# Performance work log

Hardware: AMD Instinct MI355X
Metric: run time of the kernel (lower is better)

The kernel has to match this reference:

```python
import jax, jax.numpy as jnp
import numpy as np

D_MODEL = 512
N_HEADS = 8
HEAD_DIM = D_MODEL // N_HEADS
MAX_LEN = 250  # relative table has 2*MAX_LEN-1 = 499 rows
B, L = 2, 2048


def setup_inputs() -> dict:
    rng = jax.random.key(0)
    ks = jax.random.split(rng, 10)
    w = 1.0 / np.sqrt(D_MODEL)
    return {
        "query": jax.random.normal(ks[0], (B, L, D_MODEL), jnp.float32),
        "key": jax.random.normal(ks[1], (B, L, D_MODEL), jnp.float32),
        "value": jax.random.normal(ks[2], (B, L, D_MODEL), jnp.float32),
        "mask": jax.random.randint(ks[3], (B, L), 0, 2, jnp.int32),
        # weights stored as [in, out]; apply as x @ W + b (equivalent to torch Linear)
        "Wq": jax.random.normal(ks[4], (D_MODEL, D_MODEL), jnp.float32) * w,
        "bq": jnp.zeros((D_MODEL,), jnp.float32),
        "Wk": jax.random.normal(ks[5], (D_MODEL, D_MODEL), jnp.float32) * w,
        "bk": jnp.zeros((D_MODEL,), jnp.float32),
        "Wv": jax.random.normal(ks[6], (D_MODEL, D_MODEL), jnp.float32) * w,
        "bv": jnp.zeros((D_MODEL,), jnp.float32),
        "Wo": jax.random.normal(ks[7], (D_MODEL, D_MODEL), jnp.float32) * w,
        "bo": jnp.zeros((D_MODEL,), jnp.float32),
        "rel_table": jax.random.normal(ks[8], (2 * MAX_LEN - 1, HEAD_DIM), jnp.float32),
    }


def reference(query, key, value, mask, Wq, bq, Wk, bk, Wv, bv, Wo, bo, rel_table):
    b, l, d = query.shape
    hd = d // N_HEADS

    def split_heads(x):  # [b,l,d] -> [b,h,l,hd]
        return x.reshape(b, l, N_HEADS, hd).transpose(0, 2, 1, 3)

    Q = split_heads(query @ Wq + bq)
    K = split_heads(key @ Wk + bk)
    V = split_heads(value @ Wv + bv)

    scores = jnp.einsum('bhid,bhjd->bhij', Q, K) / jnp.sqrt(jnp.float32(hd))

    # relative position indices: idx[i,j] = clamp(j - i + MAX_LEN-1, 0, 2*MAX_LEN-2)
    pos = jnp.arange(l)
    idx = jnp.clip(pos[None, :] - pos[:, None] + MAX_LEN - 1, 0, 2 * MAX_LEN - 2)
    rel = rel_table[idx]  # [l, l, hd] gather
    # Shaw-style additive relative-position bias (per-pair scalar from Q . rel)
    scores = scores + jnp.einsum('bhid,ijd->bhij', Q, rel)

    # key-padding mask: [b,l] -> [b,1,1,l]
    scores = jnp.where(mask[:, None, None, :] == 0, jnp.float32(-1e10), scores)

    weights = jax.nn.softmax(scores, axis=-1)  # [b,h,l,l]
    out = jnp.einsum('bhij,bhjd->bhid', weights, V)
    out = out.transpose(0, 2, 1, 3).reshape(b, l, d)
    return out @ Wo + bo
```

## Files before the change

### kernel.cpp

```cpp
#include <hip/hip_runtime.h>
#include <math.h>

#define NREL 499
#define NREL_PAD 504
#define LDB 72
#define LDT 72

typedef __attribute__((ext_vector_type(8))) short bf16x8;
typedef __attribute__((ext_vector_type(4))) float f32x4;

__device__ __forceinline__ float bf2f(ushort x) {
  union { unsigned u; float f; } v; v.u = ((unsigned)x) << 16; return v.f;
}
__device__ __forceinline__ ushort f2bf(float x) {
  union { float f; unsigned u; } v; v.f = x;
  return (ushort)((v.u + 0x8000u) >> 16);
}
__device__ __forceinline__ ushort f2h(float x) {
  union { _Float16 h; ushort u; } v; v.h = (_Float16)x; return v.u;
}
__device__ __forceinline__ float h2f(ushort u) {
  union { _Float16 h; ushort u; } v; v.u = u; return (float)v.h;
}
__device__ __forceinline__ bf16x8 pack8(float4 a, float4 b) {
  bf16x8 r;
  r[0] = (short)f2bf(a.x); r[1] = (short)f2bf(a.y);
  r[2] = (short)f2bf(a.z); r[3] = (short)f2bf(a.w);
  r[4] = (short)f2bf(b.x); r[5] = (short)f2bf(b.y);
  r[6] = (short)f2bf(b.z); r[7] = (short)f2bf(b.w);
  return r;
}

__global__ __launch_bounds__(256) void prep_wt(const float* __restrict__ W0,
                                               const float* __restrict__ W1,
                                               const float* __restrict__ W2,
                                               const float* __restrict__ W3,
                                               const int* __restrict__ mask,
                                               const float* __restrict__ rel,
                                               ushort* __restrict__ Wt,
                                               ushort* __restrict__ maskbf,
                                               ushort* __restrict__ rel8) {
  __shared__ float T[64][68];
  const int t = threadIdx.x;
  const int k0 = blockIdx.x * 64, n0 = blockIdx.y * 64, z = blockIdx.z;
  const float* W = (z == 0) ? W0 : (z == 1) ? W1 : (z == 2) ? W2 : W3;
#pragma unroll
  for (int s = 0; s < 4; ++s) {
    int idx = t + s * 256;
    int r = idx >> 4, c4 = (idx & 15) << 2;
    *(float4*)&T[r][c4] = *(const float4*)(W + (size_t)(k0 + r) * 512 + n0 + c4);
  }
  if (blockIdx.x == 0 && blockIdx.y == 0) {
    int base = z * 1024 + t * 4;
    int4 mv = *(const int4*)(mask + base);
    ushort4 mo;
    mo.x = mv.x ? 0x3F80 : 0; mo.y = mv.y ? 0x3F80 : 0;
    mo.z = mv.z ? 0x3F80 : 0; mo.w = mv.w ? 0x3F80 : 0;
    *(ushort4*)(maskbf + base) = mo;
  } else if (blockIdx.x == 1 && blockIdx.y == 0) {
    int base = z * 8192 + t * 32;
#pragma unroll
    for (int c = 0; c < 4; ++c) {
      int e0 = base + c * 8;
      ushort tmp[8];
#pragma unroll
      for (int k = 0; k < 8; ++k) {
        int e = e0 + k;
        float v = (e < NREL * 64) ? rel[e] * 8.f : 0.f;
        tmp[k] = f2bf(v);
      }
      *(ushort4*)(rel8 + e0) = make_ushort4(tmp[0], tmp[1], tmp[2], tmp[3]);
      *(ushort4*)(rel8 + e0 + 4) = make_ushort4(tmp[4], tmp[5], tmp[6], tmp[7]);
    }
  }
  __syncthreads();
#pragma unroll
  for (int s = 0; s < 4; ++s) {
    int idx = t + s * 256;
    int row = idx >> 4, c4 = (idx & 15) << 2;
    ushort4 u = make_ushort4(f2bf(T[c4 + 0][row]), f2bf(T[c4 + 1][row]),
                             f2bf(T[c4 + 2][row]), f2bf(T[c4 + 3][row]));
    *(ushort4*)(Wt + (size_t)z * 262144 + (size_t)(n0 + row) * 512 + k0 + c4) = u;
  }
}

template <int MODE, int AFP32>
__device__ __forceinline__ void gemm_tile_body(const void* __restrict__ Av,
                                               const ushort* __restrict__ Wt,
                                               const float* __restrict__ bias,
                                               const int* __restrict__ mvec,
                                               void* __restrict__ outv,
                                               int bx, int by, float oscale) {
  __shared__ ushort As[64 * LDT];
  __shared__ ushort Bs[64 * LDT];
  const int t = threadIdx.x;
  const int lane = t & 63, wave = t >> 6;
  const int m16 = lane & 15, quad = lane >> 4;
  const int koff = quad << 3;
  const int i0 = by * 64, n0 = bx * 64;
  const int row0 = t >> 3, off0 = (t & 7) << 3;
  const int row1 = (t + 256) >> 3, off1 = ((t + 256) & 7) << 3;
  const ushort* Ab16 = (const ushort*)Av + (size_t)i0 * 512;
  const float*  Ab32 = (const float*)Av + (size_t)i0 * 512;
  const ushort* Bb = Wt + (size_t)n0 * 512;

  uint4 ar0, ar1;
  float4 af00, af01, af10, af11;
  if (AFP32) {
    af00 = *(const float4*)(Ab32 + (size_t)row0 * 512 + off0);
    af01 = *(const float4*)(Ab32 + (size_t)row0 * 512 + off0 + 4);
    af10 = *(const float4*)(Ab32 + (size_t)row1 * 512 + off1);
    af11 = *(const float4*)(Ab32 + (size_t)row1 * 512 + off1 + 4);
  } else {
    ar0 = *(const uint4*)(Ab16 + (size_t)row0 * 512 + off0);
    ar1 = *(const uint4*)(Ab16 + (size_t)row1 * 512 + off1);
  }
  uint4 br0 = *(const uint4*)(Bb + (size_t)row0 * 512 + off0);
  uint4 br1 = *(const uint4*)(Bb + (size_t)row1 * 512 + off1);

  f32x4 acc[4] = {{0.f, 0.f, 0.f, 0.f}, {0.f, 0.f, 0.f, 0.f},
                  {0.f, 0.f, 0.f, 0.f}, {0.f, 0.f, 0.f, 0.f}};

  for (int ks = 0; ks < 8; ++ks) {
    __syncthreads();
    if (AFP32) {
      *(bf16x8*)&As[row0 * LDT + off0] = pack8(af00, af01);
      *(bf16x8*)&As[row1 * LDT + off1] = pack8(af10, af11);
    } else {
      *(uint4*)&As[row0 * LDT + off0] = ar0;
      *(uint4*)&As[row1 * LDT + off1] = ar1;
    }
    *(uint4*)&Bs[row0 * LDT + off0] = br0;
    *(uint4*)&Bs[row1 * LDT + off1] = br1;
    __syncthreads();

    const int kn = ((ks + 1) & 7) << 6;
    if (AFP32) {
      af00 = *(const float4*)(Ab32 + (size_t)row0 * 512 + kn + off0);
      af01 = *(const float4*)(Ab32 + (size_t)row0 * 512 + kn + off0 + 4);
      af10 = *(const float4*)(Ab32 + (size_t)row1 * 512 + kn + off1);
      af11 = *(const float4*)(Ab32 + (size_t)row1 * 512 + kn + off1 + 4);
    } else {
      ar0 = *(const uint4*)(Ab16 + (size_t)row0 * 512 + kn + off0);
      ar1 = *(const uint4*)(Ab16 + (size_t)row1 * 512 + kn + off1);
    }
    br0 = *(const uint4*)(Bb + (size_t)row0 * 512 + kn + off0);
    br1 = *(const uint4*)(Bb + (size_t)row1 * 512 + kn + off1);

    __builtin_amdgcn_s_setprio(1);
    if (MODE != 1) {
#pragma unroll
      for (int kh = 0; kh < 2; ++kh) {
        bf16x8 af = *(const bf16x8*)&As[((wave << 4) + m16) * LDT + (kh << 5) + koff];
#pragma unroll
        for (int nt = 0; nt < 4; ++nt) {
          bf16x8 wf = *(const bf16x8*)&Bs[((nt << 4) + m16) * LDT + (kh << 5) + koff];
          acc[nt] = __builtin_amdgcn_mfma_f32_16x16x32_bf16(af, wf, acc[nt], 0, 0, 0);
        }
      }
    } else {
#pragma unroll
      for (int kh = 0; kh < 2; ++kh) {
        bf16x8 wf = *(const bf16x8*)&Bs[((wave << 4) + m16) * LDT + (kh << 5) + koff];
#pragma unroll
        for (int it = 0; it < 4; ++it) {
          bf16x8 af = *(const bf16x8*)&As[((it << 4) + m16) * LDT + (kh << 5) + koff];
          acc[it] = __builtin_amdgcn_mfma_f32_16x16x32_bf16(wf, af, acc[it], 0, 0, 0);
        }
      }
    }
    __builtin_amdgcn_s_setprio(0);
  }

  if (MODE == 0) {
    float* out = (float*)outv;
#pragma unroll
    for (int nt = 0; nt < 4; ++nt) {
      float bn = bias[n0 + (nt << 4) + m16];
#pragma unroll
      for (int r = 0; r < 4; ++r) {
        int i = i0 + (wave << 4) + (quad << 2) + r;
        out[(size_t)i * 512 + n0 + (nt << 4) + m16] = acc[nt][r] + bn;
      }
    }
  } else {
    ushort* out = (ushort*)outv;
    const int b = i0 >> 11, l0 = i0 & 2047, h = n0 >> 6;
    float4 b4 = *(const float4*)(bias + n0 + (wave << 4) + (quad << 2));
    float bb[4] = {b4.x, b4.y, b4.z, b4.w};
    float mkf[4];
#pragma unroll
    for (int it = 0; it < 4; ++it)
      mkf[it] = (mvec[b * 2048 + l0 + (it << 4) + m16] != 0) ? 1.f : 0.f;
#pragma unroll
    for (int r = 0; r < 4; ++r) {
      int d = (wave << 4) + (quad << 2) + r;
#pragma unroll
      for (int it = 0; it < 4; ++it) {
        out[((size_t)(b * 8 + h) * 64 + d) * 2048 + l0 + (it << 4) + m16] =
            f2bf((acc[it][r] + bb[r]) * mkf[it]);
      }
    }
  }
}

template <int MODE, int AFP32>
__global__ __launch_bounds__(256) void gemm_tile(const void* __restrict__ A,
                                                 const ushort* __restrict__ Wt,
                                                 const float* __restrict__ bias,
                                                 void* __restrict__ outv) {
  gemm_tile_body<MODE, AFP32>(A, Wt, bias, nullptr, outv, blockIdx.x,
                              blockIdx.y, 1.f);
}

__device__ __forceinline__ void gemm_qk128(const float* __restrict__ A,
                                           const ushort* __restrict__ Wt,
                                           const float* __restrict__ bias,
                                           ushort* __restrict__ out,
                                           int bx, int by, float oscale) {
  __shared__ ushort As[128 * LDT];
  __shared__ ushort Bs[64 * LDT];
  const int t = threadIdx.x;
  const int lane = t & 63, wave = t >> 6;
  const int m16 = lane & 15, quad = lane >> 4;
  const int koff = quad << 3;
  const int i0 = by * 128, n0 = bx * 64;
  const float* Ab = A + (size_t)i0 * 512;
  const ushort* Bb = Wt + (size_t)n0 * 512;

  int arow[4], acol[4];
#pragma unroll
  for (int s = 0; s < 4; ++s) {
    int idx = t + s * 256;
    arow[s] = idx >> 3;
    acol[s] = (idx & 7) << 3;
  }
  const int brow0 = t >> 3, bcol0 = (t & 7) << 3;
  const int brow1 = (t + 256) >> 3, bcol1 = ((t + 256) & 7) << 3;

  float4 afA[4], afB[4];
  uint4 br0, br1;
#pragma unroll
  for (int s = 0; s < 4; ++s) {
    afA[s] = *(const float4*)(Ab + (size_t)arow[s] * 512 + acol[s]);
    afB[s] = *(const float4*)(Ab + (size_t)arow[s] * 512 + acol[s] + 4);
  }
  br0 = *(const uint4*)(Bb + (size_t)brow0 * 512 + bcol0);
  br1 = *(const uint4*)(Bb + (size_t)brow1 * 512 + bcol1);

  f32x4 acc[2][4];
#pragma unroll
  for (int mi = 0; mi < 2; ++mi)
#pragma unroll
    for (int nt = 0; nt < 4; ++nt) acc[mi][nt] = (f32x4){0.f, 0.f, 0.f, 0.f};

  for (int ks = 0; ks < 8; ++ks) {
    __syncthreads();
#pragma unroll
    for (int s = 0; s < 4; ++s)
      *(bf16x8*)&As[arow[s] * LDT + acol[s]] = pack8(afA[s], afB[s]);
    *(uint4*)&Bs[brow0 * LDT + bcol0] = br0;
    *(uint4*)&Bs[brow1 * LDT + bcol1] = br1;
    __syncthreads();

    const int kn = ((ks + 1) & 7) << 6;
#pragma unroll
    for (int s = 0; s < 4; ++s) {
      afA[s] = *(const float4*)(Ab + (size_t)arow[s] * 512 + kn + acol[s]);
      afB[s] = *(const float4*)(Ab + (size_t)arow[s] * 512 + kn + acol[s] + 4);
    }
    br0 = *(const uint4*)(Bb + (size_t)brow0 * 512 + kn + bcol0);
    br1 = *(const uint4*)(Bb + (size_t)brow1 * 512 + kn + bcol1);

    __builtin_amdgcn_s_setprio(1);
#pragma unroll
    for (int kh = 0; kh < 2; ++kh) {
      bf16x8 af0 = *(const bf16x8*)&As[((wave << 5) + m16) * LDT + (kh << 5) + koff];
      bf16x8 af1 = *(const bf16x8*)&As[((wave << 5) + 16 + m16) * LDT + (kh << 5) + koff];
#pragma unroll
      for (int nt = 0; nt < 4; ++nt) {
        bf16x8 wf = *(const bf16x8*)&Bs[((nt << 4) + m16) * LDT + (kh << 5) + koff];
        acc[0][nt] = __builtin_amdgcn_mfma_f32_16x16x32_bf16(af0, wf, acc[0][nt], 0, 0, 0);
        acc[1][nt] = __builtin_amdgcn_mfma_f32_16x16x32_bf16(af1, wf, acc[1][nt], 0, 0, 0);
      }
    }
    __builtin_amdgcn_s_setprio(0);
  }

  const int b = i0 >> 11, l0 = i0 & 2047, h = n0 >> 6;
#pragma unroll
  for (int nt = 0; nt < 4; ++nt) {
    float bn = bias[n0 + (nt << 4) + m16];
    int d = (nt << 4) + m16;
#pragma unroll
    for (int mi = 0; mi < 2; ++mi) {
#pragma unroll
      for (int r = 0; r < 4; ++r) {
        int il = (wave << 5) + (mi << 4) + (quad << 2) + r;
        out[((size_t)(b * 8 + h) * 2048 + l0 + il) * 64 + d] =
            f2bf((acc[mi][nt][r] + bn) * oscale);
      }
    }
  }
}

__global__ __launch_bounds__(256) void gemm_qkv(
    const float* __restrict__ q, const float* __restrict__ k,
    const float* __restrict__ v, const ushort* __restrict__ Wt,
    const float* __restrict__ bq, const float* __restrict__ bk,
    const float* __restrict__ bv, const int* __restrict__ mask,
    ushort* __restrict__ Qw, ushort* __restrict__ Kw, ushort* __restrict__ Vtw) {
  const int z = blockIdx.z;
  if (z == 0) {
    gemm_qk128(q, Wt, bq, Qw, blockIdx.x, blockIdx.y, 0.125f);
  } else if (z == 1) {
    gemm_qk128(k, Wt + 262144, bk, Kw, blockIdx.x, blockIdx.y, 1.f);
  } else {
#pragma unroll
    for (int s = 0; s < 2; ++s)
      gemm_tile_body<1, 1>(v, Wt + 2 * 262144, bv, mask, (void*)Vtw,
                           blockIdx.x, blockIdx.y * 2 + s, 1.f);
  }
}

__global__ __launch_bounds__(256) void qrel_tile(const ushort* __restrict__ Qw,
                                                 const ushort* __restrict__ rel8,
                                                 ushort* __restrict__ qrelh) {
  __shared__ ushort As[64 * LDT];
  __shared__ ushort Bs[64 * LDT];
  const int t = threadIdx.x;
  const int lane = t & 63, wave = t >> 6;
  const int m16 = lane & 15, quad = lane >> 4;
  const int koff = quad << 3;
  const int r0 = blockIdx.x * 64;
  const int i0 = blockIdx.y * 64;
  const int bh = blockIdx.z;
  const int row0 = t >> 3, off0 = (t & 7) << 3;
  const int row1 = (t + 256) >> 3, off1 = ((t + 256) & 7) << 3;

  *(uint4*)&As[row0 * LDT + off0] =
      *(const uint4*)(Qw + ((size_t)bh * 2048 + i0 + row0) * 64 + off0);
  *(uint4*)&As[row1 * LDT + off1] =
      *(const uint4*)(Qw + ((size_t)bh * 2048 + i0 + row1) * 64 + off1);
  *(uint4*)&Bs[row0 * LDT + off0] =
      *(const uint4*)(rel8 + (size_t)(r0 + row0) * 64 + off0);
  *(uint4*)&Bs[row1 * LDT + off1] =
      *(const uint4*)(rel8 + (size_t)(r0 + row1) * 64 + off1);
  __syncthreads();

  f32x4 acc[4] = {{0.f, 0.f, 0.f, 0.f}, {0.f, 0.f, 0.f, 0.f},
                  {0.f, 0.f, 0.f, 0.f}, {0.f, 0.f, 0.f, 0.f}};
#pragma unroll
  for (int kh = 0; kh < 2; ++kh) {
    bf16x8 af = *(const bf16x8*)&As[((wave << 4) + m16) * LDT + (kh << 5) + koff];
#pragma unroll
    for (int nt = 0; nt < 4; ++nt) {
      bf16x8 wf = *(const bf16x8*)&Bs[((nt << 4) + m16) * LDT + (kh << 5) + koff];
      acc[nt] = __builtin_amdgcn_mfma_f32_16x16x32_bf16(af, wf, acc[nt], 0, 0, 0);
    }
  }

  __syncthreads();
#pragma unroll
  for (int nt = 0; nt < 4; ++nt) {
#pragma unroll
    for (int rg = 0; rg < 4; ++rg) {
      int il = (wave << 4) + (quad << 2) + rg;
      As[il * LDT + (nt << 4) + m16] = f2h(acc[nt][rg]);
    }
  }
  __syncthreads();

  const int orow = t >> 2, och = (t & 3) << 4;
  uint4 s0 = *(const uint4*)&As[orow * LDT + och];
  uint4 s1 = *(const uint4*)&As[orow * LDT + och + 8];
  ushort* dst = qrelh + ((size_t)bh * 2048 + i0 + orow) * NREL_PAD + r0 + och;
  *(uint4*)dst = s0;
  if (r0 + och + 15 < NREL_PAD) *(uint4*)(dst + 8) = s1;
}

__device__ __forceinline__ void gather_qv(float qv[4][4],
                                          const ushort* __restrict__ qrow,
                                          float e_lo, float e_hi,
                                          int iq, int iw0, int j0, int quad) {
  if (j0 - iw0 >= 264) {
#pragma unroll
    for (int jt = 0; jt < 4; ++jt)
#pragma unroll
      for (int r = 0; r < 4; ++r) qv[jt][r] = e_hi;
  } else if (iw0 - j0 >= 312) {
#pragma unroll
    for (int jt = 0; jt < 4; ++jt)
#pragma unroll
      for (int r = 0; r < 4; ++r) qv[jt][r] = e_lo;
  } else {
#pragma unroll
    for (int jt = 0; jt < 4; ++jt) {
#pragma unroll
      for (int r = 0; r < 4; ++r) {
        int j = j0 + (jt << 4) + (quad << 2) + r;
        int rr = min(NREL - 1, max(0, j - iq + 249));
        qv[jt][r] = h2f(qrow[rr]);
      }
    }
  }
}

__global__ __launch_bounds__(256) void flash_attn(
    const ushort* __restrict__ Qw, const ushort* __restrict__ Kw,
    const ushort* __restrict__ Vt, const ushort* __restrict__ qrelh,
    const ushort* __restrict__ maskbf, ushort* __restrict__ attnbf) {
  __shared__ ushort QPs[64 * LDB];
  __shared__ ushort Ks[64 * LDB];
  __shared__ ushort Vs[64 * LDB];
  const int t = threadIdx.x;
  const int lane = t & 63, wave = t >> 6;
  const int m16 = lane & 15, quad = lane >> 4;
  const int koff = quad << 3;
  const int bid = ((int)blockIdx.y << 5) + (int)blockIdx.x;
  const int swz = ((bid & 7) << 6) + (bid >> 3);
  const int i0 = (swz & 31) << 6;
  const int bh = swz >> 5;
  const int b = bh >> 3, h = bh & 7;
  const ushort* Qb = Qw + (size_t)bh * 2048 * 64;
  const ushort* Kb = Kw + (size_t)bh * 2048 * 64;
  const ushort* Vb = Vt + (size_t)bh * 64 * 2048;
  const ushort* mbf = maskbf + b * 2048;
  const int iw0 = i0 + (wave << 4);
  const int iq = iw0 + m16;
  const ushort* qrow = qrelh + ((size_t)bh * 2048 + iq) * NREL_PAD;
  const float e_lo = h2f(qrow[0]), e_hi = h2f(qrow[NREL - 1]);

  const int row0 = t >> 3, off0 = (t & 7) << 3;
  const int row1 = (t + 256) >> 3, off1 = ((t + 256) & 7) << 3;

  *(uint4*)&QPs[row0 * LDB + off0] =
      *(const uint4*)(Qb + (size_t)(i0 + row0) * 64 + off0);
  *(uint4*)&QPs[row1 * LDB + off1] =
      *(const uint4*)(Qb + (size_t)(i0 + row1) * 64 + off1);
  __syncthreads();

  bf16x8 qa0 = *(const bf16x8*)&QPs[((wave << 4) + m16) * LDB + koff];
  bf16x8 qa1 = *(const bf16x8*)&QPs[((wave << 4) + m16) * LDB + 32 + koff];

  float m_i = -INFINITY;
  f32x4 oacc[4];
  f32x4 lacc = {0.f, 0.f, 0.f, 0.f};
#pragma unroll
  for (int dt = 0; dt < 4; ++dt) oacc[dt] = (f32x4){0.f, 0.f, 0.f, 0.f};

  uint4 krA0 = *(const uint4*)(Kb + (size_t)row0 * 64 + off0);
  uint4 krA1 = *(const uint4*)(Kb + (size_t)row1 * 64 + off1);
  uint4 vrA0 = *(const uint4*)(Vb + (size_t)row0 * 2048 + off0);
  uint4 vrA1 = *(const uint4*)(Vb + (size_t)row1 * 2048 + off1);
  bf16x8 mfA0 = *(const bf16x8*)(mbf + koff);
  bf16x8 mfA1 = *(const bf16x8*)(mbf + 32 + koff);
  float qvA[4][4];
  gather_qv(qvA, qrow, e_lo, e_hi, iq, iw0, 0, quad);
  uint4 krB0, krB1, vrB0, vrB1;
  bf16x8 mfB0, mfB1;
  float qvB[4][4];

#define FLASH_STEP(KR0, KR1, VR0, VR1, MF0, MF1, QV,                          \
                   KN0, KN1, VN0, VN1, MG0, MG1, QN, JN)                      \
  do {                                                                        \
    __syncthreads();                                                          \
    *(uint4*)&Ks[row0 * LDB + off0] = KR0;                                    \
    *(uint4*)&Ks[row1 * LDB + off1] = KR1;                                    \
    *(uint4*)&Vs[row0 * LDB + off0] = VR0;                                    \
    *(uint4*)&Vs[row1 * LDB + off1] = VR1;                                    \
    __syncthreads();                                                          \
    KN0 = *(const uint4*)(Kb + (size_t)((JN) + row0) * 64 + off0);            \
    KN1 = *(const uint4*)(Kb + (size_t)((JN) + row1) * 64 + off1);            \
    VN0 = *(const uint4*)(Vb + (size_t)row0 * 2048 + (JN) + off0);            \
    VN1 = *(const uint4*)(Vb + (size_t)row1 * 2048 + (JN) + off1);            \
    MG0 = *(const bf16x8*)(mbf + (JN) + koff);                                \
    MG1 = *(const bf16x8*)(mbf + (JN) + 32 + koff);                           \
    gather_qv(QN, qrow, e_lo, e_hi, iq, iw0, (JN), quad);                     \
    f32x4 sacc[4];                                                            \
    __builtin_amdgcn_s_setprio(1);                                            \
    _Pragma("unroll")                                                         \
    for (int jt = 0; jt < 4; ++jt) {                                          \
      bf16x8 kf0 = *(const bf16x8*)&Ks[((jt << 4) + m16) * LDB + koff];       \
      bf16x8 kf1 = *(const bf16x8*)&Ks[((jt << 4) + m16) * LDB + 32 + koff];  \
      f32x4 z = {QV[jt][0], QV[jt][1], QV[jt][2], QV[jt][3]};                 \
      z = __builtin_amdgcn_mfma_f32_16x16x32_bf16(kf0, qa0, z, 0, 0, 0);      \
      z = __builtin_amdgcn_mfma_f32_16x16x32_bf16(kf1, qa1, z, 0, 0, 0);      \
      sacc[jt] = z;                                                           \
    }                                                                         \
    __builtin_amdgcn_s_setprio(0);                                            \
    float t0 = fmaxf(fmaxf(sacc[0][0], sacc[0][1]),                           \
                     fmaxf(sacc[0][2], sacc[0][3]));                          \
    float t1 = fmaxf(fmaxf(sacc[1][0], sacc[1][1]),                           \
                     fmaxf(sacc[1][2], sacc[1][3]));                          \
    float t2 = fmaxf(fmaxf(sacc[2][0], sacc[2][1]),                           \
                     fmaxf(sacc[2][2], sacc[2][3]));                          \
    float t3 = fmaxf(fmaxf(sacc[3][0], sacc[3][1]),                           \
                     fmaxf(sacc[3][2], sacc[3][3]));                          \
    float mx = fmaxf(fmaxf(t0, t1), fmaxf(t2, t3));                           \
    mx = fmaxf(mx, __shfl_xor(mx, 16));                                       \
    mx = fmaxf(mx, __shfl_xor(mx, 32));                                       \
    if (__any(mx > m_i + 8.f)) {                                              \
      float mnew = fmaxf(m_i, mx);                                            \
      float al = __expf(m_i - mnew);                                          \
      m_i = mnew;                                                             \
      _Pragma("unroll")                                                       \
      for (int dt = 0; dt < 4; ++dt) {                                        \
        oacc[dt][0] *= al; oacc[dt][1] *= al;                                 \
        oacc[dt][2] *= al; oacc[dt][3] *= al;                                 \
      }                                                                       \
      lacc[0] *= al; lacc[1] *= al; lacc[2] *= al; lacc[3] *= al;             \
    }                                                                         \
    const int prow = ((wave << 4) + m16) * LDB;                               \
    _Pragma("unroll")                                                         \
    for (int jt = 0; jt < 4; ++jt) {                                          \
      ushort4 pk;                                                             \
      pk.x = f2bf(__expf(sacc[jt][0] - m_i));                                 \
      pk.y = f2bf(__expf(sacc[jt][1] - m_i));                                 \
      pk.z = f2bf(__expf(sacc[jt][2] - m_i));                                 \
      pk.w = f2bf(__expf(sacc[jt][3] - m_i));                                 \
      *(ushort4*)&QPs[prow + (jt << 4) + (quad << 2)] = pk;                   \
    }                                                                         \
    __asm__ volatile("s_waitcnt lgkmcnt(0)" ::: "memory");                    \
    bf16x8 pa0 = *(const bf16x8*)&QPs[prow + koff];                           \
    bf16x8 pa1 = *(const bf16x8*)&QPs[prow + 32 + koff];                      \
    __builtin_amdgcn_s_setprio(1);                                            \
    lacc = __builtin_amdgcn_mfma_f32_16x16x32_bf16(MF0, pa0, lacc, 0, 0, 0);  \
    lacc = __builtin_amdgcn_mfma_f32_16x16x32_bf16(MF1, pa1, lacc, 0, 0, 0);  \
    _Pragma("unroll")                                                         \
    for (int dt = 0; dt < 4; ++dt) {                                          \
      bf16x8 vf0 = *(const bf16x8*)&Vs[((dt << 4) + m16) * LDB + koff];       \
      bf16x8 vf1 = *(const bf16x8*)&Vs[((dt << 4) + m16) * LDB + 32 + koff];  \
      oacc[dt] =                                                              \
          __builtin_amdgcn_mfma_f32_16x16x32_bf16(vf0, pa0, oacc[dt], 0, 0, 0); \
      oacc[dt] =                                                              \
          __builtin_amdgcn_mfma_f32_16x16x32_bf16(vf1, pa1, oacc[dt], 0, 0, 0); \
    }                                                                         \
    __builtin_amdgcn_s_setprio(0);                                            \
  } while (0)

  for (int j0 = 0; j0 < 2048; j0 += 128) {
    FLASH_STEP(krA0, krA1, vrA0, vrA1, mfA0, mfA1, qvA,
               krB0, krB1, vrB0, vrB1, mfB0, mfB1, qvB, j0 + 64);
    FLASH_STEP(krB0, krB1, vrB0, vrB1, mfB0, mfB1, qvB,
               krA0, krA1, vrA0, vrA1, mfA0, mfA1, qvA, (j0 + 128) & 2047);
  }
#undef FLASH_STEP

  float inv = 1.0f / lacc[0];
  ushort* dst = attnbf + (size_t)(b * 2048 + iq) * 512 + h * 64;
#pragma unroll
  for (int dt = 0; dt < 4; ++dt) {
    ushort4 st;
    st.x = f2bf(oacc[dt][0] * inv);
    st.y = f2bf(oacc[dt][1] * inv);
    st.z = f2bf(oacc[dt][2] * inv);
    st.w = f2bf(oacc[dt][3] * inv);
    *(ushort4*)(dst + (dt << 4) + (quad << 2)) = st;
  }
}

extern "C" void kernel_launch(void* const* d_in, const int* in_sizes, int n_in,
                              void* d_out, int out_size, void* d_ws,
                              size_t ws_size, hipStream_t stream) {
  const float* query = (const float*)d_in[0];
  const float* key   = (const float*)d_in[1];
  const float* value = (const float*)d_in[2];
  const int*   mask  = (const int*)d_in[3];
  const float* Wq = (const float*)d_in[4];
  const float* bq = (const float*)d_in[5];
  const float* Wk = (const float*)d_in[6];
  const float* bk = (const float*)d_in[7];
  const float* Wv = (const float*)d_in[8];
  const float* bv = (const float*)d_in[9];
  const float* Wo = (const float*)d_in[10];
  const float* bo = (const float*)d_in[11];
  const float* rel = (const float*)d_in[12];

  char* w = (char*)d_ws;
  size_t off = 0;
  ushort* Qw  = (ushort*)(w + off); off += (size_t)16 * 2048 * 64 * 2;
  ushort* Kw  = (ushort*)(w + off); off += (size_t)16 * 2048 * 64 * 2;
  ushort* Vtw = (ushort*)(w + off); off += (size_t)16 * 64 * 2048 * 2;
  ushort* Wt  = (ushort*)(w + off); off += (size_t)4 * 512 * 512 * 2;
  ushort* qrelh = (ushort*)(w + off); off += (size_t)16 * 2048 * NREL_PAD * 2;
  ushort* attnbf = (ushort*)(w + off); off += (size_t)4096 * 512 * 2;
  ushort* maskbf = (ushort*)(w + off); off += (size_t)2 * 2048 * 2;
  ushort* rel8 = (ushort*)(w + off); off += (size_t)512 * 64 * 2;
  float* out = (float*)d_out;

  dim3 bb(256);
  hipLaunchKernelGGL(prep_wt, dim3(8, 8, 4), bb, 0, stream, Wq, Wk, Wv, Wo,
                     mask, rel, Wt, maskbf, rel8);
  hipLaunchKernelGGL(gemm_qkv, dim3(8, 32, 3), bb, 0, stream, query, key, value,
                     Wt, bq, bk, bv, mask, Qw, Kw, Vtw);
  hipLaunchKernelGGL(qrel_tile, dim3(8, 32, 16), bb, 0, stream, Qw, rel8, qrelh);
  hipLaunchKernelGGL(flash_attn, dim3(32, 16), bb, 0, stream, Qw, Kw, Vtw,
                     qrelh, maskbf, attnbf);
  hipLaunchKernelGGL((gemm_tile<0, 0>), dim3(8, 64), bb, 0, stream, attnbf,
                     Wt + 3 * 262144, bo, (void*)out);
}
```

Measured before the change: 213.8 us.

## Fuse Q·rel bias GEMM into the Q projection epilogue

Removes the separate qrel_tile kernel. The Q-projection blocks now stage their bf16 Q tile in shared memory and multiply it against the relative-position table with MFMA, writing the fp16 qrelh scores directly. This saves a kernel launch and the re-read of Q from global memory. In exchange, the 256 Q blocks take on all of the qrelh output work, which unbalances them against the K and V blocks. Their stores are also narrow 2-byte strided writes instead of the earlier LDS-staged 16-byte coalesced stores.

```diff
diff --git a/kernel.cpp b/kernel.cpp
--- a/kernel.cpp
+++ b/kernel.cpp
@@ -213,10 +213,13 @@
                               blockIdx.y, 1.f);
 }
 
+template <int QREL>
 __device__ __forceinline__ void gemm_qk128(const float* __restrict__ A,
                                            const ushort* __restrict__ Wt,
                                            const float* __restrict__ bias,
                                            ushort* __restrict__ out,
+                                           const ushort* __restrict__ rel8,
+                                           ushort* __restrict__ qrelh,
                                            int bx, int by, float oscale) {
   __shared__ ushort As[128 * LDT];
   __shared__ ushort Bs[64 * LDT];
@@ -297,8 +300,40 @@
 #pragma unroll
       for (int r = 0; r < 4; ++r) {
         int il = (wave << 5) + (mi << 4) + (quad << 2) + r;
-        out[((size_t)(b * 8 + h) * 2048 + l0 + il) * 64 + d] =
-            f2bf((acc[mi][nt][r] + bn) * oscale);
+        ushort qb = f2bf((acc[mi][nt][r] + bn) * oscale);
+        out[((size_t)(b * 8 + h) * 2048 + l0 + il) * 64 + d] = qb;
+        if (QREL) As[il * LDT + d] = qb;
+      }
+    }
+  }
+
+  if (QREL) {
+    __asm__ volatile("s_waitcnt lgkmcnt(0)" ::: "memory");
+    bf16x8 afq[2][2];
+#pragma unroll
+    for (int g = 0; g < 2; ++g)
+#pragma unroll
+      for (int kh = 0; kh < 2; ++kh)
+        afq[g][kh] = *(const bf16x8*)&As[((wave << 5) + (g << 4) + m16) * LDT +
+                                         (kh << 5) + koff];
+    const int bh = b * 8 + h;
+    for (int rc = 0; rc < 32; ++rc) {
+      const ushort* rp = rel8 + (size_t)((rc << 4) + m16) * 64;
+      bf16x8 wf0 = *(const bf16x8*)(rp + koff);
+      bf16x8 wf1 = *(const bf16x8*)(rp + 32 + koff);
+      int r = (rc << 4) + m16;
+#pragma unroll
+      for (int g = 0; g < 2; ++g) {
+        f32x4 aq = {0.f, 0.f, 0.f, 0.f};
+        aq = __builtin_amdgcn_mfma_f32_16x16x32_bf16(afq[g][0], wf0, aq, 0, 0, 0);
+        aq = __builtin_amdgcn_mfma_f32_16x16x32_bf16(afq[g][1], wf1, aq, 0, 0, 0);
+        if (r < NREL_PAD) {
+#pragma unroll
+          for (int rg = 0; rg < 4; ++rg) {
+            int l = l0 + (wave << 5) + (g << 4) + (quad << 2) + rg;
+            qrelh[((size_t)bh * 2048 + l) * NREL_PAD + r] = f2h(aq[rg]);
+          }
+        }
       }
     }
   }
@@ -309,74 +344,21 @@
     const float* __restrict__ v, const ushort* __restrict__ Wt,
     const float* __restrict__ bq, const float* __restrict__ bk,
     const float* __restrict__ bv, const int* __restrict__ mask,
-    ushort* __restrict__ Qw, ushort* __restrict__ Kw, ushort* __restrict__ Vtw) {
+    const ushort* __restrict__ rel8, ushort* __restrict__ Qw,
+    ushort* __restrict__ Kw, ushort* __restrict__ Vtw,
+    ushort* __restrict__ qrelh) {
   const int z = blockIdx.z;
   if (z == 0) {
-    gemm_qk128(q, Wt, bq, Qw, blockIdx.x, blockIdx.y, 0.125f);
+    gemm_qk128<1>(q, Wt, bq, Qw, rel8, qrelh, blockIdx.x, blockIdx.y, 0.125f);
   } else if (z == 1) {
-    gemm_qk128(k, Wt + 262144, bk, Kw, blockIdx.x, blockIdx.y, 1.f);
+    gemm_qk128<0>(k, Wt + 262144, bk, Kw, nullptr, nullptr, blockIdx.x,
+                  blockIdx.y, 1.f);
   } else {
 #pragma unroll
     for (int s = 0; s < 2; ++s)
       gemm_tile_body<1, 1>(v, Wt + 2 * 262144, bv, mask, (void*)Vtw,
                            blockIdx.x, blockIdx.y * 2 + s, 1.f);
   }
-}
-
-__global__ __launch_bounds__(256) void qrel_tile(const ushort* __restrict__ Qw,
-                                                 const ushort* __restrict__ rel8,
-                                                 ushort* __restrict__ qrelh) {
-  __shared__ ushort As[64 * LDT];
-  __shared__ ushort Bs[64 * LDT];
-  const int t = threadIdx.x;
-  const int lane = t & 63, wave = t >> 6;
-  const int m16 = lane & 15, quad = lane >> 4;
-  const int koff = quad << 3;
-  const int r0 = blockIdx.x * 64;
-  const int i0 = blockIdx.y * 64;
-  const int bh = blockIdx.z;
-  const int row0 = t >> 3, off0 = (t & 7) << 3;
-  const int row1 = (t + 256) >> 3, off1 = ((t + 256) & 7) << 3;
-
-  *(uint4*)&As[row0 * LDT + off0] =
-      *(const uint4*)(Qw + ((size_t)bh * 2048 + i0 + row0) * 64 + off0);
-  *(uint4*)&As[row1 * LDT + off1] =
-      *(const uint4*)(Qw + ((size_t)bh * 2048 + i0 + row1) * 64 + off1);
-  *(uint4*)&Bs[row0 * LDT + off0] =
-      *(const uint4*)(rel8 + (size_t)(r0 + row0) * 64 + off0);
-  *(uint4*)&Bs[row1 * LDT + off1] =
-      *(const uint4*)(rel8 + (size_t)(r0 + row1) * 64 + off1);
-  __syncthreads();
-
-  f32x4 acc[4] = {{0.f, 0.f, 0.f, 0.f}, {0.f, 0.f, 0.f, 0.f},
-                  {0.f, 0.f, 0.f, 0.f}, {0.f, 0.f, 0.f, 0.f}};
-#pragma unroll
-  for (int kh = 0; kh < 2; ++kh) {
-    bf16x8 af = *(const bf16x8*)&As[((wave << 4) + m16) * LDT + (kh << 5) + koff];
-#pragma unroll
-    for (int nt = 0; nt < 4; ++nt) {
-      bf16x8 wf = *(const bf16x8*)&Bs[((nt << 4) + m16) * LDT + (kh << 5) + koff];
-      acc[nt] = __builtin_amdgcn_mfma_f32_16x16x32_bf16(af, wf, acc[nt], 0, 0, 0);
-    }
-  }
-
-  __syncthreads();
-#pragma unroll
-  for (int nt = 0; nt < 4; ++nt) {
-#pragma unroll
-    for (int rg = 0; rg < 4; ++rg) {
-      int il = (wave << 4) + (quad << 2) + rg;
-      As[il * LDT + (nt << 4) + m16] = f2h(acc[nt][rg]);
-    }
-  }
-  __syncthreads();
-
-  const int orow = t >> 2, och = (t & 3) << 4;
-  uint4 s0 = *(const uint4*)&As[orow * LDT + och];
-  uint4 s1 = *(const uint4*)&As[orow * LDT + och + 8];
-  ushort* dst = qrelh + ((size_t)bh * 2048 + i0 + orow) * NREL_PAD + r0 + och;
-  *(uint4*)dst = s0;
-  if (r0 + och + 15 < NREL_PAD) *(uint4*)(dst + 8) = s1;
 }
 
 __device__ __forceinline__ void gather_qv(float qv[4][4],
@@ -593,8 +575,7 @@
   hipLaunchKernelGGL(prep_wt, dim3(8, 8, 4), bb, 0, stream, Wq, Wk, Wv, Wo,
                      mask, rel, Wt, maskbf, rel8);
   hipLaunchKernelGGL(gemm_qkv, dim3(8, 32, 3), bb, 0, stream, query, key, value,
-                     Wt, bq, bk, bv, mask, Qw, Kw, Vtw);
-  hipLaunchKernelGGL(qrel_tile, dim3(8, 32, 16), bb, 0, stream, Qw, rel8, qrelh);
+                     Wt, bq, bk, bv, mask, rel8, Qw, Kw, Vtw, qrelh);
   hipLaunchKernelGGL(flash_attn, dim3(32, 16), bb, 0, stream, Qw, Kw, Vtw,
                      qrelh, maskbf, attnbf);
   hipLaunchKernelGGL((gemm_tile<0, 0>), dim3(8, 64), bb, 0, stream, attnbf,
```

Result: faster. 205.5 us (-3.9%).
